# Performance work log

Hardware: AMD Instinct MI355X
Metric: run time of the kernel (lower is better)

Reference implementation:

```python
import jax, jax.numpy as jnp
import numpy as np

B = 512      # batch per stream
L = 600      # audio length (22 chunks of 75, step 25)
DIM = 256    # model dim
H = 8        # num heads (each head is full-width, per original code)
CH = [1, DIM // 4, DIM // 2, DIM]
KS = [26, 26, 25]
EPS = 1e-5
N_CHUNKS, CHUNK, STEP = 22, 75, 25


def setup_inputs() -> dict:
    key = jax.random.key(0)
    ks = iter(jax.random.split(key, 40))
    def rn(shape, scale=0.05):
        return jax.random.normal(next(ks), shape, jnp.float32) * scale
    inp = {}
    inp["audio_vec1"] = jax.random.normal(next(ks), (B, 1, L), jnp.float32)
    inp["audio_vec2"] = jax.random.normal(next(ks), (B, 1, L), jnp.float32)
    for i in range(3):
        inp[f"conv_w{i+1}"] = rn((CH[i + 1], CH[i], KS[i]))  # OIH, torch Conv1d layout
        inp[f"conv_b{i+1}"] = rn((CH[i + 1],))
        inp[f"bn_g{i+1}"] = jnp.ones((CH[i + 1],), jnp.float32)
        inp[f"bn_b{i+1}"] = jnp.zeros((CH[i + 1],), jnp.float32)
        inp[f"bn_m{i+1}"] = rn((CH[i + 1],))
        inp[f"bn_v{i+1}"] = jnp.ones((CH[i + 1],), jnp.float32)
    # per-head Q/K/V projections (stored [H, in, out]; torch Linear is x @ W.T + b)
    inp["Wq"] = rn((H, DIM, DIM)); inp["bq"] = rn((H, DIM))
    inp["Wk"] = rn((H, DIM, DIM)); inp["bk"] = rn((H, DIM))
    inp["Wv"] = rn((H, DIM, DIM)); inp["bv"] = rn((H, DIM))
    inp["fca_w"] = rn((H * DIM, DIM)); inp["fca_b"] = rn((DIM,))
    inp["fc_w"] = rn((DIM, DIM)); inp["fc_b"] = rn((DIM,))
    return inp


def _chunks(x):
    # x: [B, 1, L] -> [B*22, 1, 75] (batched chunks, chunk-major within each example)
    idx = jnp.arange(N_CHUNKS)[:, None] * STEP + jnp.arange(CHUNK)[None, :]  # [22, 75]
    c = x[:, :, idx]                      # [B, 1, 22, 75]
    return c.transpose(0, 2, 1, 3).reshape(-1, 1, CHUNK)


def _block(x, w, b, g, bt, m, v):
    # Conv1d (valid) + BatchNorm (eval) + Swish; dropout is identity in eval.
    y = jax.lax.conv_general_dilated(
        x, w, window_strides=(1,), padding="VALID",
        dimension_numbers=("NCH", "OIH", "NCH")) + b[None, :, None]
    scale = g * jax.lax.rsqrt(v + EPS)
    y = (y - m[None, :, None]) * scale[None, :, None] + bt[None, :, None]
    return y * jax.nn.sigmoid(y)


def _forward(audio_vec1, audio_vec2,
             conv_w1, conv_b1, bn_g1, bn_b1, bn_m1, bn_v1,
             conv_w2, conv_b2, bn_g2, bn_b2, bn_m2, bn_v2,
             conv_w3, conv_b3, bn_g3, bn_b3, bn_m3, bn_v3,
             Wq, bq, Wk, bk, Wv, bv, fca_w, fca_b, fc_w, fc_b):
    # Batch both streams and all 22 chunks through one conv stack.
    X = jnp.concatenate([_chunks(audio_vec1), _chunks(audio_vec2)], axis=0)  # [2*B*22,1,75]
    X = _block(X, conv_w1, conv_b1, bn_g1, bn_b1, bn_m1, bn_v1)  # [., 64, 50]
    X = _block(X, conv_w2, conv_b2, bn_g2, bn_b2, bn_m2, bn_v2)  # [., 128, 25]
    X = _block(X, conv_w3, conv_b3, bn_g3, bn_b3, bn_m3, bn_v3)  # [., 256, 1]
    feat = X[:, :, 0].reshape(-1, N_CHUNKS, DIM)  # [2B, 22, 256]

    # Multi-head attention: 8 independent full-width heads, no 1/sqrt(d) scaling.
    Q = jnp.einsum("bse,heo->bhso", feat, Wq) + bq[None, :, None, :]
    K = jnp.einsum("bse,heo->bhso", feat, Wk) + bk[None, :, None, :]
    V = jnp.einsum("bse,heo->bhso", feat, Wv) + bv[None, :, None, :]
    A = jax.nn.softmax(jnp.einsum("bhso,bhto->bhst", Q, K), axis=-1)
    O = jnp.einsum("bhst,bhto->bhso", A, V)          # [2B, H, 22, 256]
    O = O.transpose(0, 2, 1, 3).reshape(O.shape[0], N_CHUNKS, H * DIM)
    out = O @ fca_w + fca_b                            # [2B, 22, 256]

    pooled = out.mean(axis=1)                          # [2B, 256]
    y = pooled @ fc_w + fc_b                           # [2B, 256]
    nb = audio_vec1.shape[0]
    return y[:nb], y[nb:]


def reference(audio_vec1, audio_vec2,
              conv_w1, conv_b1, bn_g1, bn_b1, bn_m1, bn_v1,
              conv_w2, conv_b2, bn_g2, bn_b2, bn_m2, bn_v2,
              conv_w3, conv_b3, bn_g3, bn_b3, bn_m3, bn_v3,
              Wq, bq, Wk, bk, Wv, bv, fca_w, fca_b, fc_w, fc_b):
    return _forward(audio_vec1, audio_vec2,
                    conv_w1, conv_b1, bn_g1, bn_b1, bn_m1, bn_v1,
                    conv_w2, conv_b2, bn_g2, bn_b2, bn_m2, bn_v2,
                    conv_w3, conv_b3, bn_g3, bn_b3, bn_m3, bn_v3,
                    Wq, bq, Wk, bk, Wv, bv, fca_w, fca_b, fc_w, fc_b)
```

## Files before the change

kernel.cpp:

```cpp
#include <hip/hip_runtime.h>
#include <hip/hip_bf16.h>
#include <math.h>

#define NSEQ 22528
#define HALFSEQ 11264

typedef __attribute__((ext_vector_type(8))) short short8;
typedef __attribute__((ext_vector_type(4))) float f32x4;
typedef __attribute__((ext_vector_type(4))) ushort ushort4v;

__device__ __forceinline__ ushort f2bf(float x) {
    __hip_bfloat16 h = __float2bfloat16(x);
    return *reinterpret_cast<ushort*>(&h);
}
__device__ __forceinline__ float bf2f(ushort u) {
    unsigned v = ((unsigned)u) << 16;
    return *reinterpret_cast<float*>(&v);
}

__global__ __launch_bounds__(256) void k_prep_misc(
    const float* __restrict__ w2, ushort* __restrict__ w2f,
    const float* __restrict__ w3, ushort* __restrict__ w3f,
    const float* __restrict__ Wk, float* __restrict__ WkT,
    const float* __restrict__ bq, float* __restrict__ kb,
    const float* __restrict__ bv, const float* __restrict__ fca_w,
    const float* __restrict__ fca_b, float* __restrict__ bvc,
    const float* __restrict__ Wv, float* __restrict__ F)
{
    __shared__ float smem[16 * 256];
    const int bid = blockIdx.x;
    const int tid = threadIdx.x;

    if (bid < 832) {
        int idx = bid * 256 + tid;
        if (idx < 212992) {
            int j = idx & 7;
            int lane = (idx >> 3) & 63;
            int mt = (idx >> 9) & 7;
            int kt = idx >> 12;
            int oc = mt * 16 + (lane & 15);
            int k = kt * 32 + ((lane >> 4) << 3) + j;
            int t = k >> 6;
            int ic = k & 63;
            w2f[idx] = f2bf(w2[(oc * 64 + ic) * 26 + t]);
        }
    } else if (bid < 4032) {
        int idx = (bid - 832) * 256 + tid;
        if (idx < 819200) {
            int j = idx & 7;
            int lane = (idx >> 3) & 63;
            int mt = (idx >> 9) & 15;
            int kt = idx >> 13;
            int oc = mt * 16 + (lane & 15);
            int k = kt * 32 + ((lane >> 4) << 3) + j;
            int ic = k & 127;
            int pos = k >> 7;
            w3f[idx] = f2bf(w3[oc * 3200 + ic * 25 + pos]);
        }
    } else if (bid < 6080) {
        int idx = (bid - 4032) * 256 + tid;
        int b = idx >> 16;
        int rem = idx & 65535;
        int c = rem >> 8;
        int r = rem & 255;
        WkT[idx] = Wk[(size_t)(b * 256 + r) * 256 + c];
    } else if (bid < 6088) {
        int h = bid - 6080;
        smem[tid] = bq[h * 256 + tid];
        __syncthreads();
        const float* wk = Wk + (size_t)(h * 256 + tid) * 256;
        float a = 0.f;
        for (int o = 0; o < 256; ++o) a += wk[o] * smem[o];
        kb[h * 256 + tid] = a;
    } else if (bid < 6089) {
        for (int i = tid; i < 2048; i += 256) smem[i] = bv[i];
        __syncthreads();
        float acc = fca_b[tid];
        for (int k = 0; k < 2048; ++k) acc += smem[k] * fca_w[(size_t)k * 256 + tid];
        bvc[tid] = acc;
    } else {
        int lb = bid - 6089;
        int h = lb >> 4;
        int e0 = (lb & 15) * 16;
        for (int idx = tid; idx < 4096; idx += 256) {
            int r = idx >> 8;
            int c = idx & 255;
            smem[r * 256 + c] = Wv[(size_t)h * 65536 + (e0 + r) * 256 + c];
        }
        __syncthreads();
        float acc[16];
        #pragma unroll
        for (int r = 0; r < 16; ++r) acc[r] = 0.f;
        for (int o = 0; o < 256; ++o) {
            float w = fca_w[(size_t)(h * 256 + o) * 256 + tid];
            #pragma unroll
            for (int r = 0; r < 16; ++r) acc[r] += smem[r * 256 + o] * w;
        }
        #pragma unroll
        for (int r = 0; r < 16; ++r)
            F[(size_t)(h * 256 + e0 + r) * 256 + tid] = acc[r];
    }
}

__global__ __launch_bounds__(256) void k_prep_attn_m(
    const float* __restrict__ Wq, const float* __restrict__ WkT,
    float* __restrict__ M)
{
    const int h = blockIdx.x >> 4;
    const int e0 = (blockIdx.x & 15) * 16;
    const int tid = threadIdx.x;
    __shared__ float sq[16][256];
    for (int idx = tid; idx < 4096; idx += 256) {
        int r = idx >> 8;
        int c = idx & 255;
        sq[r][c] = Wq[(size_t)(h * 256 + e0 + r) * 256 + c];
    }
    __syncthreads();
    float acc[16];
    #pragma unroll
    for (int r = 0; r < 16; ++r) acc[r] = 0.f;
    const float* wkt = WkT + (size_t)h * 65536 + tid;
    for (int o = 0; o < 256; ++o) {
        float wk = wkt[o * 256];
        #pragma unroll
        for (int r = 0; r < 16; ++r) acc[r] += sq[r][o] * wk;
    }
    #pragma unroll
    for (int r = 0; r < 16; ++r)
        M[(size_t)(h * 256 + e0 + r) * 256 + tid] = acc[r];
}

__global__ void k_prep_mfrag(const float* __restrict__ M, ushort* __restrict__ Mfrag) {
    int idx = blockIdx.x * 256 + threadIdx.x;
    int j = idx & 7;
    int lane = (idx >> 3) & 63;
    int mt = (idx >> 9) & 15;
    int kt = (idx >> 13) & 7;
    int h = idx >> 16;
    int e = kt * 32 + ((lane >> 4) << 3) + j;
    int o = mt * 16 + (lane & 15);
    Mfrag[idx] = f2bf(M[(size_t)(h * 256 + e) * 256 + o]);
}

__global__ __launch_bounds__(512, 4) void k_conv(
    const float* __restrict__ av1, const float* __restrict__ av2,
    const float* __restrict__ w1,
    const float* __restrict__ b1c, const float* __restrict__ g1,
    const float* __restrict__ be1, const float* __restrict__ m1, const float* __restrict__ v1,
    const ushort* __restrict__ w2f,
    const float* __restrict__ b2c, const float* __restrict__ g2,
    const float* __restrict__ be2, const float* __restrict__ m2, const float* __restrict__ v2,
    ushort* __restrict__ a2f, int seqoff)
{
    __shared__ ushort s_a1[8 * 3200];
    __shared__ ushort s_w1f[2048];
    __shared__ ushort s_xb[8][80];
    __shared__ float s_sc1[64], s_sh1[64], s_sc2[128], s_sh2[128];

    const int tid = threadIdx.x;
    const int lane = tid & 63;
    const int w = tid >> 6;
    const int l15 = lane & 15;
    const int grp = lane >> 4;
    const int lseq0 = blockIdx.x * 8;
    const int gseq0 = seqoff + lseq0;

    for (int idx = tid; idx < 640; idx += 512) {
        int s = idx / 80;
        int i = idx - s * 80;
        int seq = gseq0 + s;
        const float* src;
        if (seq < HALFSEQ) { int b = seq / 22; int n = seq - b * 22; src = av1 + b * 600 + n * 25; }
        else { int q = seq - HALFSEQ; int b = q / 22; int n = q - b * 22; src = av2 + b * 600 + n * 25; }
        s_xb[s][i] = f2bf((i < 75) ? src[i] : 0.f);
    }
    for (int idx = tid; idx < 2048; idx += 512) {
        int j = idx & 7;
        int ln = (idx >> 3) & 63;
        int mt = idx >> 9;
        int oc = mt * 16 + (ln & 15);
        int k = ((ln >> 4) << 3) + j;
        s_w1f[idx] = (k < 26) ? f2bf(w1[oc * 26 + k]) : (ushort)0;
    }
    if (tid < 64) { float A = g1[tid] * rsqrtf(v1[tid] + 1e-5f); s_sc1[tid] = A; s_sh1[tid] = (b1c[tid] - m1[tid]) * A + be1[tid]; }
    if (tid >= 128 && tid < 256) {
        int o = tid - 128;
        float A = g2[o] * rsqrtf(v2[o] + 1e-5f); s_sc2[o] = A; s_sh2[o] = (b2c[o] - m2[o]) * A + be2[o];
    }
    __syncthreads();

    {
        short8 a1f[4];
        #pragma unroll
        for (int mt = 0; mt < 4; ++mt)
            a1f[mt] = *(const short8*)(s_w1f + mt * 512 + lane * 8);

        for (int nt = w; nt < 25; nt += 8) {
            int n = nt * 16 + l15;
            int s = n / 50;
            int p = n - s * 50;
            short8 bf;
            #pragma unroll
            for (int j = 0; j < 8; ++j) {
                int t = grp * 8 + j;
                bf[j] = (t < 26) ? (short)s_xb[s][p + t] : (short)0;
            }
            #pragma unroll
            for (int mt = 0; mt < 4; ++mt) {
                f32x4 acc1 = (f32x4){0.f, 0.f, 0.f, 0.f};
                acc1 = __builtin_amdgcn_mfma_f32_16x16x32_bf16(a1f[mt], bf, acc1, 0, 0, 0);
                int oc0 = mt * 16 + grp * 4;
                int icb = oc0 >> 3;
                int boff = s * 6400 + icb * 800 + p * 16 + (oc0 & 7) * 2;
                ushort4v u;
                #pragma unroll
                for (int r = 0; r < 4; ++r) {
                    float y = acc1[r] * s_sc1[oc0 + r] + s_sh1[oc0 + r];
                    y = y / (1.f + __expf(-y));
                    u[r] = f2bf(y);
                }
                *(ushort4v*)((char*)s_a1 + boff) = u;
            }
        }
    }
    __syncthreads();

    {
        const int mset = w & 3;
        const int nset = w >> 2;
        const int NT = nset ? 6 : 7;

        int vaddr[7];
        #pragma unroll
        for (int ni = 0; ni < 7; ++ni) {
            int nt = nset * 7 + ni;
            int n = nt * 16 + l15;
            int s = n / 25; if (s > 7) s = 7;
            int p = n - s * 25; if (p > 24) p = 24;
            vaddr[ni] = s * 6400 + grp * 800 + p * 16;
        }

        f32x4 acc[2][7];
        #pragma unroll
        for (int mi = 0; mi < 2; ++mi)
            #pragma unroll
            for (int ni = 0; ni < 7; ++ni)
                acc[mi][ni] = (f32x4){0.f, 0.f, 0.f, 0.f};

        const ushort* wpt = w2f + (size_t)(mset * 2) * 512 + lane * 8;
        short8 afA0 = *(const short8*)(wpt);
        short8 afA1 = *(const short8*)(wpt + 512);
        short8 afB0 = *(const short8*)(wpt + 4096);
        short8 afB1 = *(const short8*)(wpt + 4096 + 512);

        for (int t = 0; t < 26; ++t) {
            #pragma unroll
            for (int ni = 0; ni < 7; ++ni) {
                if (ni >= NT) break;
                short8 bf = *(const short8*)((const char*)s_a1 + vaddr[ni]);
                acc[0][ni] = __builtin_amdgcn_mfma_f32_16x16x32_bf16(afA0, bf, acc[0][ni], 0, 0, 0);
                acc[1][ni] = __builtin_amdgcn_mfma_f32_16x16x32_bf16(afA1, bf, acc[1][ni], 0, 0, 0);
            }
            if (t < 25) {
                afA0 = *(const short8*)(wpt + 8192);
                afA1 = *(const short8*)(wpt + 8192 + 512);
            }
            #pragma unroll
            for (int ni = 0; ni < 7; ++ni) {
                if (ni >= NT) break;
                short8 bf = *(const short8*)((const char*)s_a1 + vaddr[ni] + 3200);
                acc[0][ni] = __builtin_amdgcn_mfma_f32_16x16x32_bf16(afB0, bf, acc[0][ni], 0, 0, 0);
                acc[1][ni] = __builtin_amdgcn_mfma_f32_16x16x32_bf16(afB1, bf, acc[1][ni], 0, 0, 0);
            }
            if (t < 25) {
                afB0 = *(const short8*)(wpt + 12288);
                afB1 = *(const short8*)(wpt + 12288 + 512);
                wpt += 8192;
            }
            #pragma unroll
            for (int ni = 0; ni < 7; ++ni) vaddr[ni] += 16;
        }

        #pragma unroll
        for (int mi = 0; mi < 2; ++mi) {
            const int ocb = mset * 32 + mi * 16 + grp * 4;
            const int grp_dst = (ocb >> 3) & 3;
            const int jb = ocb & 7;
            const int kthi = ocb >> 5;
            #pragma unroll
            for (int ni = 0; ni < 7; ++ni) {
                if (ni >= NT) break;
                int n = (nset * 7 + ni) * 16 + l15;
                if (n < 200) {
                    int s = n / 25;
                    int p = n - s * 25;
                    int seq = lseq0 + s;
                    int kt3 = p * 4 + kthi;
                    ushort4v u;
                    #pragma unroll
                    for (int r = 0; r < 4; ++r) {
                        float y = acc[mi][ni][r] * s_sc2[ocb + r] + s_sh2[ocb + r];
                        y = y / (1.f + __expf(-y));
                        u[r] = f2bf(y);
                    }
                    *(ushort4v*)(a2f + (((size_t)(seq >> 4) * 100 + kt3) << 9)
                                 + ((seq & 15) + 16 * grp_dst) * 8 + jb) = u;
                }
            }
        }
    }
}

__global__ __launch_bounds__(256) void k_conv3(
    const ushort* __restrict__ a2f, const ushort* __restrict__ w3f,
    const float* __restrict__ b3c, const float* __restrict__ g3,
    const float* __restrict__ be3, const float* __restrict__ m3, const float* __restrict__ v3,
    float* __restrict__ feat, int seqoff)
{
    const int tid = threadIdx.x;
    const int lane = tid & 63;
    const int wv = tid >> 6;
    const int l15 = lane & 15;
    const int grp = lane >> 4;
    const int lseq0 = blockIdx.x * 64;

    f32x4 acc3[4][4];
    #pragma unroll
    for (int mi = 0; mi < 4; ++mi)
        #pragma unroll
        for (int nt = 0; nt < 4; ++nt)
            acc3[mi][nt] = (f32x4){0.f, 0.f, 0.f, 0.f};

    const ushort* bp = a2f + ((size_t)(lseq0 >> 4) * 100) * 512 + lane * 8;
    const ushort* ap = w3f + (size_t)(wv * 4) * 512 + lane * 8;

    for (int kt = 0; kt < 100; ++kt) {
        short8 bf[4];
        #pragma unroll
        for (int nt = 0; nt < 4; ++nt)
            bf[nt] = *(const short8*)(bp + (size_t)(nt * 100 + kt) * 512);
        #pragma unroll
        for (int mi = 0; mi < 4; ++mi) {
            short8 af = *(const short8*)(ap + (size_t)kt * 8192 + mi * 512);
            #pragma unroll
            for (int nt = 0; nt < 4; ++nt)
                acc3[mi][nt] = __builtin_amdgcn_mfma_f32_16x16x32_bf16(af, bf[nt], acc3[mi][nt], 0, 0, 0);
        }
    }

    #pragma unroll
    for (int nt = 0; nt < 4; ++nt) {
        int gseq = seqoff + lseq0 + nt * 16 + l15;
        #pragma unroll
        for (int mi = 0; mi < 4; ++mi) {
            int oc = wv * 64 + mi * 16 + grp * 4;
            float4 o4;
            #pragma unroll
            for (int r = 0; r < 4; ++r) {
                float A = g3[oc + r] * rsqrtf(v3[oc + r] + 1e-5f);
                float y = acc3[mi][nt][r] * A + (b3c[oc + r] - m3[oc + r]) * A + be3[oc + r];
                ((float*)&o4)[r] = y / (1.f + __expf(-y));
            }
            *(float4*)(feat + (size_t)gseq * 256 + oc) = o4;
        }
    }
}

__global__ __launch_bounds__(256, 2) void k_attn_f(
    const float* __restrict__ feat, const ushort* __restrict__ Mfrag,
    const float* __restrict__ kb, float* __restrict__ fbar_all)
{
    const int g = blockIdx.x;
    const int tid = threadIdx.x;
    const int lane = tid & 63;
    const int wv = tid >> 6;
    const int l15 = lane & 15;
    const int grp = lane >> 4;

    __shared__ __align__(16) float sfL[22 * 260];
    __shared__ __align__(16) ushort sfb[32 * 256];
    __shared__ __align__(16) ushort sG[32 * 256];
    __shared__ float sS[22 * 24];
    __shared__ float sbet[8][24];
    __shared__ float sab[24];

    const float* fsrc = feat + (size_t)g * 5632;
    for (int idx = tid; idx < 8192; idx += 256) {
        int s = idx >> 8;
        int e = idx & 255;
        float f = 0.f;
        if (s < 22) { f = fsrc[s * 256 + e]; sfL[s * 260 + e] = f; }
        int byte = s * 512 + ((e * 2) ^ ((s & 7) << 4));
        *(ushort*)((char*)sfb + byte) = f2bf(f);
    }
    __syncthreads();

    if (tid < 176) {
        int t = tid >> 3;
        int h = tid & 7;
        const float* kr = kb + h * 256;
        const float* fr = sfL + t * 260;
        float a = 0.f;
        for (int e = 0; e < 256; ++e) a += fr[e] * kr[e];
        sbet[h][t] = a;
    }
    __syncthreads();

    for (int h = 0; h < 8; ++h) {
        {
            f32x4 accg[2][4];
            #pragma unroll
            for (int mt = 0; mt < 2; ++mt)
                #pragma unroll
                for (int fi = 0; fi < 4; ++fi)
                    accg[mt][fi] = (f32x4){0.f, 0.f, 0.f, 0.f};

            const ushort* mfb = Mfrag + (size_t)h * 65536;
            for (int kt = 0; kt < 8; ++kt) {
                int e0b = (kt * 32 + grp * 8) * 2;
                int rA0 = l15, rA1 = 16 + l15;
                short8 af0 = *(const short8*)((const char*)sfb + rA0 * 512 + (e0b ^ ((rA0 & 7) << 4)));
                short8 af1 = *(const short8*)((const char*)sfb + rA1 * 512 + (e0b ^ ((rA1 & 7) << 4)));
                #pragma unroll
                for (int fi = 0; fi < 4; ++fi) {
                    int ft = wv * 4 + fi;
                    short8 bfm = *(const short8*)(mfb + (size_t)((kt * 16 + ft) << 9) + lane * 8);
                    accg[0][fi] = __builtin_amdgcn_mfma_f32_16x16x32_bf16(af0, bfm, accg[0][fi], 0, 0, 0);
                    accg[1][fi] = __builtin_amdgcn_mfma_f32_16x16x32_bf16(af1, bfm, accg[1][fi], 0, 0, 0);
                }
            }
            #pragma unroll
            for (int mt = 0; mt < 2; ++mt) {
                #pragma unroll
                for (int fi = 0; fi < 4; ++fi) {
                    int f = (wv * 4 + fi) * 16 + l15;
                    #pragma unroll
                    for (int r = 0; r < 4; ++r) {
                        int s = mt * 16 + grp * 4 + r;
                        if (s < 22) {
                            int byte = s * 512 + ((f * 2) ^ ((s & 7) << 4));
                            *(ushort*)((char*)sG + byte) = f2bf(accg[mt][fi][r]);
                        }
                    }
                }
            }
        }
        __syncthreads();

        {
            int mt2 = wv >> 1;
            int nt2 = wv & 1;
            f32x4 sacc = (f32x4){0.f, 0.f, 0.f, 0.f};
            int sA = mt2 * 16 + l15;
            int tB = nt2 * 16 + l15;
            for (int kt = 0; kt < 8; ++kt) {
                int f0b = (kt * 32 + grp * 8) * 2;
                short8 ga = *(const short8*)((const char*)sG + sA * 512 + (f0b ^ ((sA & 7) << 4)));
                short8 fb = *(const short8*)((const char*)sfb + tB * 512 + (f0b ^ ((tB & 7) << 4)));
                sacc = __builtin_amdgcn_mfma_f32_16x16x32_bf16(ga, fb, sacc, 0, 0, 0);
            }
            #pragma unroll
            for (int r = 0; r < 4; ++r) {
                int s = mt2 * 16 + grp * 4 + r;
                int t = nt2 * 16 + l15;
                if (s < 22 && t < 22) sS[s * 24 + t] = sacc[r] + sbet[h][t];
            }
        }
        __syncthreads();

        if (tid < 22) {
            int s = tid;
            float mx = -1e30f;
            #pragma unroll
            for (int t = 0; t < 22; ++t) mx = fmaxf(mx, sS[s * 24 + t]);
            float ex[22];
            float sum = 0.f;
            #pragma unroll
            for (int t = 0; t < 22; ++t) { float e2 = __expf(sS[s * 24 + t] - mx); ex[t] = e2; sum += e2; }
            float inv = 1.f / sum;
            #pragma unroll
            for (int t = 0; t < 22; ++t) sS[s * 24 + t] = ex[t] * inv;
        }
        __syncthreads();
        if (tid < 22) {
            int t = tid;
            float a = 0.f;
            #pragma unroll
            for (int s = 0; s < 22; ++s) a += sS[s * 24 + t];
            sab[t] = a * (1.f / 22.f);
        }
        __syncthreads();

        {
            float a = 0.f;
            #pragma unroll
            for (int t = 0; t < 22; ++t) a += sab[t] * sfL[t * 260 + tid];
            fbar_all[((size_t)g * 8 + h) * 256 + tid] = a;
        }
    }
}

__global__ __launch_bounds__(256) void k_pool(
    const float* __restrict__ fbar_all, const float* __restrict__ F,
    const float* __restrict__ bvc,
    const float* __restrict__ fc_w, const float* __restrict__ fc_b,
    float* __restrict__ out)
{
    const int g0 = blockIdx.x * 4;
    const int tid = threadIdx.x;
    __shared__ __align__(16) float sfb[32 * 256];
    __shared__ __align__(16) float sp[4 * 256];
    for (int idx = tid; idx < 8192; idx += 256)
        sfb[idx] = fbar_all[(size_t)g0 * 8 * 256 + idx];
    __syncthreads();

    float p[4];
    float bb = bvc[tid];
    #pragma unroll
    for (int j = 0; j < 4; ++j) p[j] = bb;
    for (int k = 0; k < 2048; ++k) {
        float f = F[(size_t)k * 256 + tid];
        #pragma unroll
        for (int j = 0; j < 4; ++j) p[j] += sfb[j * 2048 + k] * f;
    }
    #pragma unroll
    for (int j = 0; j < 4; ++j) sp[j * 256 + tid] = p[j];
    __syncthreads();

    float y[4];
    float fb = fc_b[tid];
    #pragma unroll
    for (int j = 0; j < 4; ++j) y[j] = fb;
    for (int e = 0; e < 256; ++e) {
        float w = fc_w[(size_t)e * 256 + tid];
        #pragma unroll
        for (int j = 0; j < 4; ++j) y[j] += sp[j * 256 + e] * w;
    }
    #pragma unroll
    for (int j = 0; j < 4; ++j)
        out[(size_t)(g0 + j) * 256 + tid] = y[j];
}

extern "C" void kernel_launch(void* const* d_in, const int* in_sizes, int n_in,
                              void* d_out, int out_size, void* d_ws, size_t ws_size,
                              hipStream_t stream) {
    (void)in_sizes; (void)n_in; (void)out_size;

    const float* av1   = (const float*)d_in[0];
    const float* av2   = (const float*)d_in[1];
    const float* w1    = (const float*)d_in[2];
    const float* b1c   = (const float*)d_in[3];
    const float* g1    = (const float*)d_in[4];
    const float* be1   = (const float*)d_in[5];
    const float* m1    = (const float*)d_in[6];
    const float* v1    = (const float*)d_in[7];
    const float* w2    = (const float*)d_in[8];
    const float* b2c   = (const float*)d_in[9];
    const float* g2    = (const float*)d_in[10];
    const float* be2   = (const float*)d_in[11];
    const float* m2    = (const float*)d_in[12];
    const float* v2    = (const float*)d_in[13];
    const float* w3    = (const float*)d_in[14];
    const float* b3c   = (const float*)d_in[15];
    const float* g3    = (const float*)d_in[16];
    const float* be3   = (const float*)d_in[17];
    const float* m3    = (const float*)d_in[18];
    const float* v3    = (const float*)d_in[19];
    const float* Wq    = (const float*)d_in[20];
    const float* bq    = (const float*)d_in[21];
    const float* Wk    = (const float*)d_in[22];
    const float* bk    = (const float*)d_in[23];
    const float* Wv    = (const float*)d_in[24];
    const float* bv    = (const float*)d_in[25];
    const float* fca_w = (const float*)d_in[26];
    const float* fca_b = (const float*)d_in[27];
    const float* fc_w  = (const float*)d_in[28];
    const float* fc_b  = (const float*)d_in[29];
    (void)bk;

    float* ws = (float*)d_ws;
    float* feat = ws;
    float* Mm   = feat + 5767168;
    float* WkT  = Mm + 524288;
    float* kb   = WkT + 524288;
    float* bvc  = kb + 2048;
    float* F    = bvc + 256;
    float* fbar = F + 524288;
    ushort* w2f = (ushort*)(fbar + 2097152);
    ushort* w3f = w2f + 212992;
    ushort* mfr = w3f + 819200;
    ushort* region = mfr + 524288;

    size_t base_bytes = (size_t)((char*)region - (char*)d_ws);
    size_t budget = (ws_size > base_bytes + 4096) ? (ws_size - base_bytes - 4096) : 0;
    int ncA = 16;
    const int cand[5] = {1, 2, 4, 8, 16};
    for (int i = 0; i < 5; ++i) { if ((size_t)144179200 / cand[i] <= budget) { ncA = cand[i]; break; } }
    const int seqsA = NSEQ / ncA;

    k_prep_misc<<<6217, 256, 0, stream>>>(w2, w2f, w3, w3f, Wk, WkT,
                                          bq, kb, bv, fca_w, fca_b, bvc, Wv, F);
    k_prep_attn_m<<<128, 256, 0, stream>>>(Wq, WkT, Mm);
    k_prep_mfrag<<<2048, 256, 0, stream>>>(Mm, mfr);

    ushort* a2f = region;
    for (int c = 0; c < ncA; ++c) {
        int seqoff = c * seqsA;
        k_conv<<<seqsA / 8, 512, 0, stream>>>(av1, av2,
            w1, b1c, g1, be1, m1, v1,
            w2f, b2c, g2, be2, m2, v2,
            a2f, seqoff);
        k_conv3<<<seqsA / 64, 256, 0, stream>>>(a2f, w3f,
            b3c, g3, be3, m3, v3, feat, seqoff);
    }

    k_attn_f<<<1024, 256, 0, stream>>>(feat, mfr, kb, fbar);
    k_pool<<<256, 256, 0, stream>>>(fbar, F, bvc, fc_w, fc_b, (float*)d_out);
}
```

Measured before the change: 601.4 us.

## Retile conv3, attention, pooling and weight-prep kernels for better reuse and parallelism

Weight fragment prep for conv2/conv3 moves to dedicated kernels that stage rows through shared memory, so global reads are coalesced. conv3 now splits the output channels across two blocks, which doubles the grid and halves the accumulators per wave. The attention kernel handles two groups per 512-thread block, computes the key-bias term with MFMA using a precomputed bf16 fragment, and drops the fp32 feature copy in favour of the bf16 shared buffer. Pooling processes eight groups per block with vectorized shared reads. The changes trade some fp32 precision in the fbar sum for lower shared memory use and more reuse of the Mfrag and F loads.

```diff
diff --git a/kernel.cpp b/kernel.cpp
--- a/kernel.cpp
+++ b/kernel.cpp
@@ -19,8 +19,6 @@
 }
 
 __global__ __launch_bounds__(256) void k_prep_misc(
-    const float* __restrict__ w2, ushort* __restrict__ w2f,
-    const float* __restrict__ w3, ushort* __restrict__ w3f,
     const float* __restrict__ Wk, float* __restrict__ WkT,
     const float* __restrict__ bq, float* __restrict__ kb,
     const float* __restrict__ bv, const float* __restrict__ fca_w,
@@ -31,55 +29,29 @@
     const int bid = blockIdx.x;
     const int tid = threadIdx.x;
 
-    if (bid < 832) {
+    if (bid < 2048) {
         int idx = bid * 256 + tid;
-        if (idx < 212992) {
-            int j = idx & 7;
-            int lane = (idx >> 3) & 63;
-            int mt = (idx >> 9) & 7;
-            int kt = idx >> 12;
-            int oc = mt * 16 + (lane & 15);
-            int k = kt * 32 + ((lane >> 4) << 3) + j;
-            int t = k >> 6;
-            int ic = k & 63;
-            w2f[idx] = f2bf(w2[(oc * 64 + ic) * 26 + t]);
-        }
-    } else if (bid < 4032) {
-        int idx = (bid - 832) * 256 + tid;
-        if (idx < 819200) {
-            int j = idx & 7;
-            int lane = (idx >> 3) & 63;
-            int mt = (idx >> 9) & 15;
-            int kt = idx >> 13;
-            int oc = mt * 16 + (lane & 15);
-            int k = kt * 32 + ((lane >> 4) << 3) + j;
-            int ic = k & 127;
-            int pos = k >> 7;
-            w3f[idx] = f2bf(w3[oc * 3200 + ic * 25 + pos]);
-        }
-    } else if (bid < 6080) {
-        int idx = (bid - 4032) * 256 + tid;
         int b = idx >> 16;
         int rem = idx & 65535;
         int c = rem >> 8;
         int r = rem & 255;
         WkT[idx] = Wk[(size_t)(b * 256 + r) * 256 + c];
-    } else if (bid < 6088) {
-        int h = bid - 6080;
+    } else if (bid < 2056) {
+        int h = bid - 2048;
         smem[tid] = bq[h * 256 + tid];
         __syncthreads();
         const float* wk = Wk + (size_t)(h * 256 + tid) * 256;
         float a = 0.f;
         for (int o = 0; o < 256; ++o) a += wk[o] * smem[o];
         kb[h * 256 + tid] = a;
-    } else if (bid < 6089) {
+    } else if (bid < 2057) {
         for (int i = tid; i < 2048; i += 256) smem[i] = bv[i];
         __syncthreads();
         float acc = fca_b[tid];
         for (int k = 0; k < 2048; ++k) acc += smem[k] * fca_w[(size_t)k * 256 + tid];
         bvc[tid] = acc;
     } else {
-        int lb = bid - 6089;
+        int lb = bid - 2057;
         int h = lb >> 4;
         int e0 = (lb & 15) * 16;
         for (int idx = tid; idx < 4096; idx += 256) {
@@ -102,6 +74,54 @@
     }
 }
 
+__global__ __launch_bounds__(256) void k_prep_w2t(
+    const float* __restrict__ w2, ushort* __restrict__ w2f)
+{
+    __shared__ float tile[13312];
+    const int mt = blockIdx.x >> 1;
+    const int ich = blockIdx.x & 1;
+    const int tid = threadIdx.x;
+    for (int idx = tid; idx < 13312; idx += 256) {
+        int oc16 = idx / 832;
+        int rem = idx - oc16 * 832;
+        tile[idx] = w2[(size_t)(mt * 16 + oc16) * 1664 + ich * 832 + rem];
+    }
+    __syncthreads();
+    for (int wi = tid; wi < 26 * 512; wi += 256) {
+        int t = wi >> 9;
+        int li = wi & 511;
+        int lane = li >> 3;
+        int j = li & 7;
+        int oc16 = lane & 15;
+        int il = ((lane >> 4) << 3) + j;
+        w2f[(size_t)(((2 * t + ich) * 8 + mt) << 9) + li] = f2bf(tile[oc16 * 832 + il * 26 + t]);
+    }
+}
+
+__global__ __launch_bounds__(256) void k_prep_w3t(
+    const float* __restrict__ w3, ushort* __restrict__ w3f)
+{
+    __shared__ float tile[12800];
+    const int mt = blockIdx.x >> 2;
+    const int icb = blockIdx.x & 3;
+    const int tid = threadIdx.x;
+    for (int idx = tid; idx < 12800; idx += 256) {
+        int oc16 = idx / 800;
+        int rem = idx - oc16 * 800;
+        tile[idx] = w3[(size_t)(mt * 16 + oc16) * 3200 + icb * 800 + rem];
+    }
+    __syncthreads();
+    for (int wi = tid; wi < 25 * 512; wi += 256) {
+        int pos = wi >> 9;
+        int li = wi & 511;
+        int lane = li >> 3;
+        int j = li & 7;
+        int oc16 = lane & 15;
+        int il = ((lane >> 4) << 3) + j;
+        w3f[(size_t)(((pos * 4 + icb) * 16 + mt) << 9) + li] = f2bf(tile[oc16 * 800 + il * 25 + pos]);
+    }
+}
+
 __global__ __launch_bounds__(256) void k_prep_attn_m(
     const float* __restrict__ Wq, const float* __restrict__ WkT,
     float* __restrict__ M)
@@ -130,16 +150,29 @@
         M[(size_t)(h * 256 + e0 + r) * 256 + tid] = acc[r];
 }
 
-__global__ void k_prep_mfrag(const float* __restrict__ M, ushort* __restrict__ Mfrag) {
-    int idx = blockIdx.x * 256 + threadIdx.x;
-    int j = idx & 7;
-    int lane = (idx >> 3) & 63;
-    int mt = (idx >> 9) & 15;
-    int kt = (idx >> 13) & 7;
-    int h = idx >> 16;
-    int e = kt * 32 + ((lane >> 4) << 3) + j;
-    int o = mt * 16 + (lane & 15);
-    Mfrag[idx] = f2bf(M[(size_t)(h * 256 + e) * 256 + o]);
+__global__ void k_prep_mfrag(const float* __restrict__ M, ushort* __restrict__ Mfrag,
+                             const float* __restrict__ kb, ushort* __restrict__ kbf) {
+    int bid = blockIdx.x;
+    int tid = threadIdx.x;
+    if (bid < 2048) {
+        int idx = bid * 256 + tid;
+        int j = idx & 7;
+        int lane = (idx >> 3) & 63;
+        int mt = (idx >> 9) & 15;
+        int kt = (idx >> 13) & 7;
+        int h = idx >> 16;
+        int e = kt * 32 + ((lane >> 4) << 3) + j;
+        int o = mt * 16 + (lane & 15);
+        Mfrag[idx] = f2bf(M[(size_t)(h * 256 + e) * 256 + o]);
+    } else {
+        int idx = (bid - 2048) * 256 + tid;
+        int j = idx & 7;
+        int lane = (idx >> 3) & 63;
+        int kt = idx >> 9;
+        int h = lane & 15;
+        int e = kt * 32 + ((lane >> 4) << 3) + j;
+        kbf[idx] = (h < 8) ? f2bf(kb[h * 256 + e]) : (ushort)0;
+    }
 }
 
 __global__ __launch_bounds__(512, 4) void k_conv(
@@ -322,17 +355,20 @@
     const int wv = tid >> 6;
     const int l15 = lane & 15;
     const int grp = lane >> 4;
-    const int lseq0 = blockIdx.x * 64;
-
-    f32x4 acc3[4][4];
-    #pragma unroll
-    for (int mi = 0; mi < 4; ++mi)
+    const int sb = blockIdx.x >> 1;
+    const int mh = blockIdx.x & 1;
+    const int lseq0 = sb * 64;
+    const int mtb = mh * 8 + wv * 2;
+
+    f32x4 acc3[2][4];
+    #pragma unroll
+    for (int mi = 0; mi < 2; ++mi)
         #pragma unroll
         for (int nt = 0; nt < 4; ++nt)
             acc3[mi][nt] = (f32x4){0.f, 0.f, 0.f, 0.f};
 
     const ushort* bp = a2f + ((size_t)(lseq0 >> 4) * 100) * 512 + lane * 8;
-    const ushort* ap = w3f + (size_t)(wv * 4) * 512 + lane * 8;
+    const ushort* ap = w3f + (size_t)mtb * 512 + lane * 8;
 
     for (int kt = 0; kt < 100; ++kt) {
         short8 bf[4];
@@ -340,7 +376,7 @@
         for (int nt = 0; nt < 4; ++nt)
             bf[nt] = *(const short8*)(bp + (size_t)(nt * 100 + kt) * 512);
         #pragma unroll
-        for (int mi = 0; mi < 4; ++mi) {
+        for (int mi = 0; mi < 2; ++mi) {
             short8 af = *(const short8*)(ap + (size_t)kt * 8192 + mi * 512);
             #pragma unroll
             for (int nt = 0; nt < 4; ++nt)
@@ -352,8 +388,8 @@
     for (int nt = 0; nt < 4; ++nt) {
         int gseq = seqoff + lseq0 + nt * 16 + l15;
         #pragma unroll
-        for (int mi = 0; mi < 4; ++mi) {
-            int oc = wv * 64 + mi * 16 + grp * 4;
+        for (int mi = 0; mi < 2; ++mi) {
+            int oc = (mtb + mi) * 16 + grp * 4;
             float4 o4;
             #pragma unroll
             for (int r = 0; r < 4; ++r) {
@@ -366,80 +402,96 @@
     }
 }
 
-__global__ __launch_bounds__(256, 2) void k_attn_f(
+__global__ __launch_bounds__(512, 2) void k_attn_f(
     const float* __restrict__ feat, const ushort* __restrict__ Mfrag,
-    const float* __restrict__ kb, float* __restrict__ fbar_all)
-{
-    const int g = blockIdx.x;
+    const ushort* __restrict__ kbf, float* __restrict__ fbar_all)
+{
+    const int g0 = blockIdx.x * 2;
     const int tid = threadIdx.x;
     const int lane = tid & 63;
     const int wv = tid >> 6;
     const int l15 = lane & 15;
     const int grp = lane >> 4;
 
-    __shared__ __align__(16) float sfL[22 * 260];
-    __shared__ __align__(16) ushort sfb[32 * 256];
-    __shared__ __align__(16) ushort sG[32 * 256];
-    __shared__ float sS[22 * 24];
-    __shared__ float sbet[8][24];
-    __shared__ float sab[24];
-
-    const float* fsrc = feat + (size_t)g * 5632;
-    for (int idx = tid; idx < 8192; idx += 256) {
-        int s = idx >> 8;
+    __shared__ __align__(16) ushort sfb[2 * 32 * 256];
+    __shared__ __align__(16) ushort sG[2 * 32 * 256];
+    __shared__ float sS[2 * 528];
+    __shared__ float sbet[2 * 192];
+    __shared__ float sab[2 * 24];
+
+    char* const sfbb = (char*)sfb;
+    char* const sGb = (char*)sG;
+
+    for (int idx = tid; idx < 16384; idx += 512) {
+        int gg = idx >> 13;
+        int s = (idx >> 8) & 31;
         int e = idx & 255;
-        float f = 0.f;
-        if (s < 22) { f = fsrc[s * 256 + e]; sfL[s * 260 + e] = f; }
-        int byte = s * 512 + ((e * 2) ^ ((s & 7) << 4));
-        *(ushort*)((char*)sfb + byte) = f2bf(f);
-    }
-    __syncthreads();
-
-    if (tid < 176) {
-        int t = tid >> 3;
-        int h = tid & 7;
-        const float* kr = kb + h * 256;
-        const float* fr = sfL + t * 260;
-        float a = 0.f;
-        for (int e = 0; e < 256; ++e) a += fr[e] * kr[e];
-        sbet[h][t] = a;
+        float f = (s < 22) ? feat[(size_t)(g0 + gg) * 5632 + s * 256 + e] : 0.f;
+        int byte = gg * 16384 + s * 512 + ((e * 2) ^ ((s & 7) << 4));
+        *(ushort*)(sfbb + byte) = f2bf(f);
+    }
+    __syncthreads();
+
+    if (wv < 4) {
+        int gg = wv >> 1;
+        int rowb = (wv & 1) * 16;
+        int rA = rowb + l15;
+        f32x4 acc = (f32x4){0.f, 0.f, 0.f, 0.f};
+        for (int kt = 0; kt < 8; ++kt) {
+            int e0b = (kt * 32 + grp * 8) * 2;
+            short8 af = *(const short8*)(sfbb + gg * 16384 + rA * 512 + (e0b ^ ((rA & 7) << 4)));
+            short8 bf = *(const short8*)(kbf + kt * 512 + lane * 8);
+            acc = __builtin_amdgcn_mfma_f32_16x16x32_bf16(af, bf, acc, 0, 0, 0);
+        }
+        #pragma unroll
+        for (int r = 0; r < 4; ++r) {
+            int t = rowb + grp * 4 + r;
+            int h = l15;
+            if (t < 22 && h < 8) sbet[gg * 192 + h * 24 + t] = acc[r];
+        }
     }
     __syncthreads();
 
     for (int h = 0; h < 8; ++h) {
         {
-            f32x4 accg[2][4];
-            #pragma unroll
-            for (int mt = 0; mt < 2; ++mt)
+            f32x4 accg[4][2];
+            #pragma unroll
+            for (int mt = 0; mt < 4; ++mt)
                 #pragma unroll
-                for (int fi = 0; fi < 4; ++fi)
+                for (int fi = 0; fi < 2; ++fi)
                     accg[mt][fi] = (f32x4){0.f, 0.f, 0.f, 0.f};
 
             const ushort* mfb = Mfrag + (size_t)h * 65536;
             for (int kt = 0; kt < 8; ++kt) {
                 int e0b = (kt * 32 + grp * 8) * 2;
-                int rA0 = l15, rA1 = 16 + l15;
-                short8 af0 = *(const short8*)((const char*)sfb + rA0 * 512 + (e0b ^ ((rA0 & 7) << 4)));
-                short8 af1 = *(const short8*)((const char*)sfb + rA1 * 512 + (e0b ^ ((rA1 & 7) << 4)));
+                short8 af[4];
                 #pragma unroll
-                for (int fi = 0; fi < 4; ++fi) {
-                    int ft = wv * 4 + fi;
+                for (int mt = 0; mt < 4; ++mt) {
+                    int gg = mt >> 1;
+                    int rA = (mt & 1) * 16 + l15;
+                    af[mt] = *(const short8*)(sfbb + gg * 16384 + rA * 512 + (e0b ^ ((rA & 7) << 4)));
+                }
+                #pragma unroll
+                for (int fi = 0; fi < 2; ++fi) {
+                    int ft = wv * 2 + fi;
                     short8 bfm = *(const short8*)(mfb + (size_t)((kt * 16 + ft) << 9) + lane * 8);
-                    accg[0][fi] = __builtin_amdgcn_mfma_f32_16x16x32_bf16(af0, bfm, accg[0][fi], 0, 0, 0);
-                    accg[1][fi] = __builtin_amdgcn_mfma_f32_16x16x32_bf16(af1, bfm, accg[1][fi], 0, 0, 0);
+                    #pragma unroll
+                    for (int mt = 0; mt < 4; ++mt)
+                        accg[mt][fi] = __builtin_amdgcn_mfma_f32_16x16x32_bf16(af[mt], bfm, accg[mt][fi], 0, 0, 0);
                 }
             }
             #pragma unroll
-            for (int mt = 0; mt < 2; ++mt) {
+            for (int mt = 0; mt < 4; ++mt) {
+                int gg = mt >> 1;
                 #pragma unroll
-                for (int fi = 0; fi < 4; ++fi) {
-                    int f = (wv * 4 + fi) * 16 + l15;
+                for (int fi = 0; fi < 2; ++fi) {
+                    int f = (wv * 2 + fi) * 16 + l15;
                     #pragma unroll
                     for (int r = 0; r < 4; ++r) {
-                        int s = mt * 16 + grp * 4 + r;
+                        int s = (mt & 1) * 16 + grp * 4 + r;
                         if (s < 22) {
-                            int byte = s * 512 + ((f * 2) ^ ((s & 7) << 4));
-                            *(ushort*)((char*)sG + byte) = f2bf(accg[mt][fi][r]);
+                            int byte = gg * 16384 + s * 512 + ((f * 2) ^ ((s & 7) << 4));
+                            *(ushort*)(sGb + byte) = f2bf(accg[mt][fi][r]);
                         }
                     }
                 }
@@ -448,55 +500,67 @@
         __syncthreads();
 
         {
-            int mt2 = wv >> 1;
+            int gg = wv >> 2;
+            int mt2 = (wv >> 1) & 1;
             int nt2 = wv & 1;
             f32x4 sacc = (f32x4){0.f, 0.f, 0.f, 0.f};
             int sA = mt2 * 16 + l15;
             int tB = nt2 * 16 + l15;
             for (int kt = 0; kt < 8; ++kt) {
                 int f0b = (kt * 32 + grp * 8) * 2;
-                short8 ga = *(const short8*)((const char*)sG + sA * 512 + (f0b ^ ((sA & 7) << 4)));
-                short8 fb = *(const short8*)((const char*)sfb + tB * 512 + (f0b ^ ((tB & 7) << 4)));
+                short8 ga = *(const short8*)(sGb + gg * 16384 + sA * 512 + (f0b ^ ((sA & 7) << 4)));
+                short8 fb = *(const short8*)(sfbb + gg * 16384 + tB * 512 + (f0b ^ ((tB & 7) << 4)));
                 sacc = __builtin_amdgcn_mfma_f32_16x16x32_bf16(ga, fb, sacc, 0, 0, 0);
             }
             #pragma unroll
             for (int r = 0; r < 4; ++r) {
                 int s = mt2 * 16 + grp * 4 + r;
                 int t = nt2 * 16 + l15;
-                if (s < 22 && t < 22) sS[s * 24 + t] = sacc[r] + sbet[h][t];
-            }
-        }
-        __syncthreads();
-
-        if (tid < 22) {
-            int s = tid;
+                if (s < 22 && t < 22)
+                    sS[gg * 528 + s * 24 + t] = sacc[r] + sbet[gg * 192 + h * 24 + t];
+            }
+        }
+        __syncthreads();
+
+        if (tid < 44) {
+            int gg = tid >= 22;
+            int s = tid - gg * 22;
+            float* row = sS + gg * 528 + s * 24;
             float mx = -1e30f;
             #pragma unroll
-            for (int t = 0; t < 22; ++t) mx = fmaxf(mx, sS[s * 24 + t]);
+            for (int t = 0; t < 22; ++t) mx = fmaxf(mx, row[t]);
             float ex[22];
             float sum = 0.f;
             #pragma unroll
-            for (int t = 0; t < 22; ++t) { float e2 = __expf(sS[s * 24 + t] - mx); ex[t] = e2; sum += e2; }
+            for (int t = 0; t < 22; ++t) { float e2 = __expf(row[t] - mx); ex[t] = e2; sum += e2; }
             float inv = 1.f / sum;
             #pragma unroll
-            for (int t = 0; t < 22; ++t) sS[s * 24 + t] = ex[t] * inv;
-        }
-        __syncthreads();
-        if (tid < 22) {
-            int t = tid;
+            for (int t = 0; t < 22; ++t) row[t] = ex[t] * inv;
+        }
+        __syncthreads();
+        if (tid < 44) {
+            int gg = tid >= 22;
+            int t = tid - gg * 22;
             float a = 0.f;
             #pragma unroll
-            for (int s = 0; s < 22; ++s) a += sS[s * 24 + t];
-            sab[t] = a * (1.f / 22.f);
+            for (int s = 0; s < 22; ++s) a += sS[gg * 528 + s * 24 + t];
+            sab[gg * 24 + t] = a * (1.f / 22.f);
         }
         __syncthreads();
 
         {
+            int gg = tid >> 8;
+            int e = tid & 255;
+            int e2b = e * 2;
             float a = 0.f;
             #pragma unroll
-            for (int t = 0; t < 22; ++t) a += sab[t] * sfL[t * 260 + tid];
-            fbar_all[((size_t)g * 8 + h) * 256 + tid] = a;
-        }
+            for (int t = 0; t < 22; ++t) {
+                ushort u = *(ushort*)(sfbb + gg * 16384 + t * 512 + (e2b ^ ((t & 7) << 4)));
+                a += sab[gg * 24 + t] * bf2f(u);
+            }
+            fbar_all[((size_t)(g0 + gg) * 8 + h) * 256 + e] = a;
+        }
+        __syncthreads();
     }
 }
 
@@ -506,38 +570,44 @@
     const float* __restrict__ fc_w, const float* __restrict__ fc_b,
     float* __restrict__ out)
 {
-    const int g0 = blockIdx.x * 4;
-    const int tid = threadIdx.x;
-    __shared__ __align__(16) float sfb[32 * 256];
-    __shared__ __align__(16) float sp[4 * 256];
-    for (int idx = tid; idx < 8192; idx += 256)
+    const int g0 = blockIdx.x * 8;
+    const int tid = threadIdx.x;
+    __shared__ __align__(16) float sfb[8 * 2048];
+    __shared__ __align__(16) float sp[8 * 256];
+    for (int idx = tid; idx < 16384; idx += 256)
         sfb[idx] = fbar_all[(size_t)g0 * 8 * 256 + idx];
     __syncthreads();
 
-    float p[4];
+    float p[8];
     float bb = bvc[tid];
     #pragma unroll
-    for (int j = 0; j < 4; ++j) p[j] = bb;
-    for (int k = 0; k < 2048; ++k) {
-        float f = F[(size_t)k * 256 + tid];
-        #pragma unroll
-        for (int j = 0; j < 4; ++j) p[j] += sfb[j * 2048 + k] * f;
-    }
-    #pragma unroll
-    for (int j = 0; j < 4; ++j) sp[j * 256 + tid] = p[j];
-    __syncthreads();
-
-    float y[4];
+    for (int j = 0; j < 8; ++j) p[j] = bb;
+    for (int k = 0; k < 2048; k += 4) {
+        float f0 = F[(size_t)(k + 0) * 256 + tid];
+        float f1 = F[(size_t)(k + 1) * 256 + tid];
+        float f2 = F[(size_t)(k + 2) * 256 + tid];
+        float f3 = F[(size_t)(k + 3) * 256 + tid];
+        #pragma unroll
+        for (int j = 0; j < 8; ++j) {
+            float4 v = *(const float4*)(sfb + j * 2048 + k);
+            p[j] += v.x * f0 + v.y * f1 + v.z * f2 + v.w * f3;
+        }
+    }
+    #pragma unroll
+    for (int j = 0; j < 8; ++j) sp[j * 256 + tid] = p[j];
+    __syncthreads();
+
+    float y[8];
     float fb = fc_b[tid];
     #pragma unroll
-    for (int j = 0; j < 4; ++j) y[j] = fb;
+    for (int j = 0; j < 8; ++j) y[j] = fb;
     for (int e = 0; e < 256; ++e) {
         float w = fc_w[(size_t)e * 256 + tid];
         #pragma unroll
-        for (int j = 0; j < 4; ++j) y[j] += sp[j * 256 + e] * w;
-    }
-    #pragma unroll
-    for (int j = 0; j < 4; ++j)
+        for (int j = 0; j < 8; ++j) y[j] += sp[j * 256 + e] * w;
+    }
+    #pragma unroll
+    for (int j = 0; j < 8; ++j)
         out[(size_t)(g0 + j) * 256 + tid] = y[j];
 }
 
@@ -589,7 +659,8 @@
     ushort* w2f = (ushort*)(fbar + 2097152);
     ushort* w3f = w2f + 212992;
     ushort* mfr = w3f + 819200;
-    ushort* region = mfr + 524288;
+    ushort* kbf = mfr + 524288;
+    ushort* region = kbf + 4096;
 
     size_t base_bytes = (size_t)((char*)region - (char*)d_ws);
     size_t budget = (ws_size > base_bytes + 4096) ? (ws_size - base_bytes - 4096) : 0;
@@ -598,10 +669,11 @@
     for (int i = 0; i < 5; ++i) { if ((size_t)144179200 / cand[i] <= budget) { ncA = cand[i]; break; } }
     const int seqsA = NSEQ / ncA;
 
-    k_prep_misc<<<6217, 256, 0, stream>>>(w2, w2f, w3, w3f, Wk, WkT,
-                                          bq, kb, bv, fca_w, fca_b, bvc, Wv, F);
+    k_prep_misc<<<2185, 256, 0, stream>>>(Wk, WkT, bq, kb, bv, fca_w, fca_b, bvc, Wv, F);
+    k_prep_w2t<<<16, 256, 0, stream>>>(w2, w2f);
+    k_prep_w3t<<<64, 256, 0, stream>>>(w3, w3f);
     k_prep_attn_m<<<128, 256, 0, stream>>>(Wq, WkT, Mm);
-    k_prep_mfrag<<<2048, 256, 0, stream>>>(Mm, mfr);
+    k_prep_mfrag<<<2064, 256, 0, stream>>>(Mm, mfr, kb, kbf);
 
     ushort* a2f = region;
     for (int c = 0; c < ncA; ++c) {
@@ -610,10 +682,10 @@
             w1, b1c, g1, be1, m1, v1,
             w2f, b2c, g2, be2, m2, v2,
             a2f, seqoff);
-        k_conv3<<<seqsA / 64, 256, 0, stream>>>(a2f, w3f,
+        k_conv3<<<(seqsA / 64) * 2, 256, 0, stream>>>(a2f, w3f,
             b3c, g3, be3, m3, v3, feat, seqoff);
     }
 
-    k_attn_f<<<1024, 256, 0, stream>>>(feat, mfr, kb, fbar);
-    k_pool<<<256, 256, 0, stream>>>(fbar, F, bvc, fc_w, fc_b, (float*)d_out);
-}
+    k_attn_f<<<512, 512, 0, stream>>>(feat, mfr, kbf, fbar);
+    k_pool<<<128, 256, 0, stream>>>(fbar, F, bvc, fc_w, fc_b, (float*)d_out);
+}
```

New measurement: 581.2 us. 1.03x faster.
